# Kernel tuning notes

Hardware: AMD Instinct MI355X
Metric: run time of the kernel (lower is better)

Reference implementation:

```python
import jax, jax.numpy as jnp
import numpy as np

H = 1024
E = 8
TOPK = 2
MLP_H = 4 * H   # resmlp hidden
EXP_H = 2 * H   # expert hidden
EPS_LN = 1e-5


def _ln(x, g, b):
    mu = jnp.mean(x, axis=-1, keepdims=True)
    var = jnp.mean(jnp.square(x - mu), axis=-1, keepdims=True)
    return (x - mu) * jax.lax.rsqrt(var + EPS_LN) * g + b


def setup_inputs() -> dict:
    key = jax.random.key(0)
    ks = jax.random.split(key, 16)
    s = 0.02
    return {
        "x": jax.random.normal(ks[0], (2, 2048, H), jnp.float32),
        # ResidualMLPBlock params
        "ln1_g": jnp.ones((H,), jnp.float32),
        "ln1_b": jnp.zeros((H,), jnp.float32),
        "ln2_g": jnp.ones((H,), jnp.float32),
        "ln2_b": jnp.zeros((H,), jnp.float32),
        "w1": jax.random.normal(ks[1], (H, MLP_H), jnp.float32) * s,
        "b1": jnp.zeros((MLP_H,), jnp.float32),
        "w2": jax.random.normal(ks[2], (MLP_H, H), jnp.float32) * s,
        "b2": jnp.zeros((H,), jnp.float32),
        # MoE params
        "router_w": jax.random.normal(ks[3], (H, E), jnp.float32) * s,
        "ew1": jax.random.normal(ks[4], (E, H, EXP_H), jnp.float32) * s,
        "eb1": jnp.zeros((E, EXP_H), jnp.float32),
        "ew2": jax.random.normal(ks[5], (E, EXP_H, H), jnp.float32) * s,
        "eb2": jnp.zeros((E, H), jnp.float32),
        # final LayerNorm
        "lnf_g": jnp.ones((H,), jnp.float32),
        "lnf_b": jnp.zeros((H,), jnp.float32),
    }


def reference(x, ln1_g, ln1_b, ln2_g, ln2_b, w1, b1, w2, b2,
              router_w, ew1, eb1, ew2, eb2, lnf_g, lnf_b):
    B, L, Hd = x.shape
    # --- ResidualMLPBlock ---
    r = x
    h = _ln(x, ln1_g, ln1_b)
    h = jax.nn.gelu(h @ w1 + b1, approximate=False) @ w2 + b2
    h = h + r
    x = _ln(h, ln2_g, ln2_b) + h
    # --- AdvancedMoEBlock (eval: no dropout / jitter) ---
    xf = x.reshape(-1, Hd)                       # [N, H]
    N = xf.shape[0]
    probs = jax.nn.softmax(xf @ router_w, axis=-1)   # [N, E]
    topk_p, topk_i = jax.lax.top_k(probs, TOPK)      # [N, K]
    topk_p = topk_p / jnp.sum(topk_p, axis=-1, keepdims=True)
    # dense combine weights: w[n, e] = sum_k topk_p[n,k] * [topk_i[n,k]==e]
    comb = jnp.zeros((N, E), xf.dtype).at[jnp.arange(N)[:, None], topk_i].add(topk_p)
    # all-experts dense compute, weighted combine (same math as masked dispatch)
    he = jax.nn.gelu(jnp.einsum('nh,ehf->enf', xf, ew1) + eb1[:, None, :],
                     approximate=False)          # [E, N, 2H]
    ye = jnp.einsum('enf,efh->enh', he, ew2) + eb2[:, None, :]  # [E, N, H]
    out = jnp.einsum('enh,ne->nh', ye, comb).reshape(B, L, Hd)
    # aux load-balancing loss
    counts = jax.ops.segment_sum(jnp.ones((N * TOPK,), jnp.float32),
                                 topk_i.reshape(-1), num_segments=E)
    load = counts / jnp.sum(counts)
    aux_loss = 0.01 * jnp.sum(load * jnp.log(load + 1e-9))
    # --- final LayerNorm ---
    out = _ln(out, lnf_g, lnf_b)
    return out, aux_loss
```

## Files before the change

kernel.cpp:

```cpp
#include <hip/hip_runtime.h>
#include <cstdint>


#define NTOK 4096
#define HD 1024
#define MLPH 4096
#define EXPH 2048
#define NEXP 8
#define KSPLIT 2
#define KCH 2048
#define MAXSLOT 9216

typedef __attribute__((ext_vector_type(8))) _Float16 f16x8;
typedef __attribute__((ext_vector_type(4))) float f32x4v;

__device__ __forceinline__ float gelu_f(float v) {
  return 0.5f * v * (1.0f + erff(v * 0.7071067811865475f));
}

__device__ __forceinline__ void load16_lds(const void* g, void* lds) {
  __builtin_amdgcn_global_load_lds(
      (__attribute__((address_space(1))) unsigned int*)(uintptr_t)g,
      (__attribute__((address_space(3))) unsigned int*)(unsigned)(uintptr_t)lds,
      16, 0, 0);
}

__global__ void transpose_conv2(const float* __restrict__ w1, const float* __restrict__ w2,
                                _Float16* __restrict__ o1, _Float16* __restrict__ o2) {
  __shared__ float t[32][33];
  int z = blockIdx.z;
  const float* in = z ? w2 : w1;
  _Float16* oh = z ? o2 : o1;
  int R = z ? MLPH : HD, C = z ? HD : MLPH;
  int c0 = (z ? blockIdx.y : blockIdx.x) * 32;
  int r0 = (z ? blockIdx.x : blockIdx.y) * 32;
  int tx = threadIdx.x & 31, ty = threadIdx.x >> 5;
#pragma unroll
  for (int i = 0; i < 4; ++i)
    t[ty + i * 8][tx] = in[(size_t)(r0 + ty + i * 8) * C + c0 + tx];
  __syncthreads();
#pragma unroll
  for (int i = 0; i < 4; ++i)
    oh[(size_t)(c0 + ty + i * 8) * R + r0 + tx] = (_Float16)t[tx][ty + i * 8];
}

__global__ void transpose_f16_2(const float* __restrict__ ew1, const float* __restrict__ ew2,
                                _Float16* __restrict__ ew1t, _Float16* __restrict__ ew2t) {
  __shared__ float t[32][33];
  int z = blockIdx.z;
  const float* in;
  _Float16* out;
  int R, C, c0, r0;
  if (z < 8) {
    in = ew1 + (size_t)z * HD * EXPH; out = ew1t + (size_t)z * HD * EXPH;
    R = HD; C = EXPH; c0 = blockIdx.x * 32; r0 = blockIdx.y * 32;
  } else {
    int e = z - 8;
    in = ew2 + (size_t)e * EXPH * HD; out = ew2t + (size_t)e * EXPH * HD;
    R = EXPH; C = HD; c0 = blockIdx.y * 32; r0 = blockIdx.x * 32;
  }
  int tx = threadIdx.x & 31, ty = threadIdx.x >> 5;
#pragma unroll
  for (int i = 0; i < 4; ++i)
    t[ty + i * 8][tx] = in[(size_t)(r0 + ty + i * 8) * C + c0 + tx];
  __syncthreads();
#pragma unroll
  for (int i = 0; i < 4; ++i)
    out[(size_t)(c0 + ty + i * 8) * R + r0 + tx] = (_Float16)t[tx][ty + i * 8];
}

__global__ void ln1_kernel(const float* __restrict__ x, const float* __restrict__ g,
                           const float* __restrict__ b, _Float16* __restrict__ oh) {
  int row = blockIdx.x, tid = threadIdx.x;
  const float4* xr = (const float4*)(x + (size_t)row * HD);
  float4 v = xr[tid];
  float s = v.x + v.y + v.z + v.w;
  float s2 = v.x * v.x + v.y * v.y + v.z * v.z + v.w * v.w;
  __shared__ float red[8];
#pragma unroll
  for (int o = 32; o > 0; o >>= 1) { s += __shfl_xor(s, o, 64); s2 += __shfl_xor(s2, o, 64); }
  if ((tid & 63) == 0) { red[tid >> 6] = s; red[(tid >> 6) + 4] = s2; }
  __syncthreads();
  s = red[0] + red[1] + red[2] + red[3];
  s2 = red[4] + red[5] + red[6] + red[7];
  float mu = s * (1.0f / HD);
  float rstd = 1.0f / sqrtf(s2 * (1.0f / HD) - mu * mu + 1e-5f);
  float4 gv = ((const float4*)g)[tid], bv = ((const float4*)b)[tid];
  size_t base = (size_t)row * HD + tid * 4;
  oh[base + 0] = (_Float16)((v.x - mu) * rstd * gv.x + bv.x);
  oh[base + 1] = (_Float16)((v.y - mu) * rstd * gv.y + bv.y);
  oh[base + 2] = (_Float16)((v.z - mu) * rstd * gv.z + bv.z);
  oh[base + 3] = (_Float16)((v.w - mu) * rstd * gv.w + bv.w);
}

__global__ __launch_bounds__(256, 2) void gemm_f16_gelu(
    const _Float16* __restrict__ A, const _Float16* __restrict__ B,
    const float* __restrict__ bias, _Float16* __restrict__ out, int N, int K) {
  int m0 = blockIdx.y * 128, n0 = blockIdx.x * 128;
  __shared__ __align__(16) _Float16 sA[128 * 64], sB[128 * 64];
  int tid = threadIdx.x, wave = tid >> 6, lane = tid & 63;
  int wm = wave >> 1, wn = wave & 1;
  int r16 = lane & 15, q = lane >> 4;
  f32x4v acc[4][4] = {};
  const _Float16* pA = A + (size_t)m0 * K;
  const _Float16* pB = B + (size_t)n0 * K;
  for (int k0 = 0; k0 < K; k0 += 64) {
    __syncthreads();
#pragma unroll
    for (int i = 0; i < 4; ++i) {
      int s = i * 256 + wave * 64 + lane;
      int row = s >> 3, c2 = s & 7;
      int c2s = c2 ^ (row & 7);
      size_t goff = (size_t)row * K + k0 + c2s * 8;
      int loff = (i * 256 + wave * 64) * 16;
      load16_lds(pA + goff, (char*)sA + loff);
      load16_lds(pB + goff, (char*)sB + loff);
    }
    __syncthreads();
#pragma unroll
    for (int ks = 0; ks < 2; ++ks) {
      f16x8 bf[4];
#pragma unroll
      for (int t = 0; t < 4; ++t) {
        int rowb = wn * 64 + t * 16 + r16;
        bf[t] = *(const f16x8*)&sB[rowb * 64 + ((ks * 4 + q) ^ (rowb & 7)) * 8];
      }
#pragma unroll
      for (int mt = 0; mt < 4; ++mt) {
        int rowa = wm * 64 + mt * 16 + r16;
        f16x8 af = *(const f16x8*)&sA[rowa * 64 + ((ks * 4 + q) ^ (rowa & 7)) * 8];
#pragma unroll
        for (int nt = 0; nt < 4; ++nt)
          acc[mt][nt] = __builtin_amdgcn_mfma_f32_16x16x32_f16(af, bf[nt], acc[mt][nt], 0, 0, 0);
      }
    }
  }
#pragma unroll
  for (int mt = 0; mt < 4; ++mt)
#pragma unroll
    for (int nt = 0; nt < 4; ++nt) {
      int col = n0 + wn * 64 + nt * 16 + r16;
      float bv = bias[col];
#pragma unroll
      for (int r = 0; r < 4; ++r) {
        size_t grow = (size_t)(m0 + wm * 64 + mt * 16 + q * 4 + r);
        out[grow * N + col] = (_Float16)gelu_f(acc[mt][nt][r] + bv);
      }
    }
}

__global__ __launch_bounds__(256, 2) void gemm_f16_pk(
    const _Float16* __restrict__ A, const _Float16* __restrict__ B,
    float* __restrict__ part, int N, int K) {
  int orig = blockIdx.x + 8 * (blockIdx.y + 32 * blockIdx.z);
  int xcd = orig & 7, idx = orig >> 3;
  int wg = xcd * 64 + idx;
  int bz = wg >> 8;
  int rr = wg & 255;
  int by = rr >> 3, bx = rr & 7;
  int m0 = by * 128, n0 = bx * 128;
  int kbase = bz * KCH;
  __shared__ __align__(16) _Float16 sA[128 * 64], sB[128 * 64];
  int tid = threadIdx.x, wave = tid >> 6, lane = tid & 63;
  int wm = wave >> 1, wn = wave & 1;
  int r16 = lane & 15, q = lane >> 4;
  f32x4v acc[4][4] = {};
  const _Float16* pA = A + (size_t)m0 * K + kbase;
  const _Float16* pB = B + (size_t)n0 * K + kbase;
  for (int k0 = 0; k0 < KCH; k0 += 64) {
    __syncthreads();
#pragma unroll
    for (int i = 0; i < 4; ++i) {
      int s = i * 256 + wave * 64 + lane;
      int row = s >> 3, c2 = s & 7;
      int c2s = c2 ^ (row & 7);
      size_t goff = (size_t)row * K + k0 + c2s * 8;
      int loff = (i * 256 + wave * 64) * 16;
      load16_lds(pA + goff, (char*)sA + loff);
      load16_lds(pB + goff, (char*)sB + loff);
    }
    __syncthreads();
#pragma unroll
    for (int ks = 0; ks < 2; ++ks) {
      f16x8 bf[4];
#pragma unroll
      for (int t = 0; t < 4; ++t) {
        int rowb = wn * 64 + t * 16 + r16;
        bf[t] = *(const f16x8*)&sB[rowb * 64 + ((ks * 4 + q) ^ (rowb & 7)) * 8];
      }
#pragma unroll
      for (int mt = 0; mt < 4; ++mt) {
        int rowa = wm * 64 + mt * 16 + r16;
        f16x8 af = *(const f16x8*)&sA[rowa * 64 + ((ks * 4 + q) ^ (rowa & 7)) * 8];
#pragma unroll
        for (int nt = 0; nt < 4; ++nt)
          acc[mt][nt] = __builtin_amdgcn_mfma_f32_16x16x32_f16(af, bf[nt], acc[mt][nt], 0, 0, 0);
      }
    }
  }
  float* pz = part + (size_t)bz * NTOK * HD;
#pragma unroll
  for (int mt = 0; mt < 4; ++mt)
#pragma unroll
    for (int nt = 0; nt < 4; ++nt) {
      int col = n0 + wn * 64 + nt * 16 + r16;
#pragma unroll
      for (int r = 0; r < 4; ++r) {
        size_t grow = (size_t)(m0 + wm * 64 + mt * 16 + q * 4 + r);
        pz[grow * N + col] = acc[mt][nt][r];
      }
    }
}

__global__ void reduce_ln2_router_kernel(
    const float* __restrict__ part, const float* __restrict__ x,
    const float* __restrict__ b2, const float* __restrict__ g,
    const float* __restrict__ b, const float* __restrict__ rw,
    _Float16* __restrict__ x2h, int* __restrict__ tidx, float* __restrict__ twt,
    int* __restrict__ counts) {
  int row = blockIdx.x, tid = threadIdx.x;
  int lane = tid & 63, wid = tid >> 6;
  float4 v = {0, 0, 0, 0};
#pragma unroll
  for (int z = 0; z < KSPLIT; ++z) {
    float4 p = ((const float4*)(part + ((size_t)z * NTOK + row) * HD))[tid];
    v.x += p.x; v.y += p.y; v.z += p.z; v.w += p.w;
  }
  float4 bb = ((const float4*)b2)[tid];
  float4 xv = ((const float4*)(x + (size_t)row * HD))[tid];
  v.x += bb.x + xv.x; v.y += bb.y + xv.y; v.z += bb.z + xv.z; v.w += bb.w + xv.w;
  float s = v.x + v.y + v.z + v.w;
  float s2 = v.x * v.x + v.y * v.y + v.z * v.z + v.w * v.w;
  __shared__ float red[8];
  __shared__ float sred[4][8];
#pragma unroll
  for (int o = 32; o > 0; o >>= 1) { s += __shfl_xor(s, o, 64); s2 += __shfl_xor(s2, o, 64); }
  if (lane == 0) { red[wid] = s; red[wid + 4] = s2; }
  __syncthreads();
  s = red[0] + red[1] + red[2] + red[3];
  s2 = red[4] + red[5] + red[6] + red[7];
  float mu = s * (1.0f / HD);
  float rstd = 1.0f / sqrtf(s2 * (1.0f / HD) - mu * mu + 1e-5f);
  float4 gv = ((const float4*)g)[tid], bv = ((const float4*)b)[tid];
  float4 o4;
  o4.x = (v.x - mu) * rstd * gv.x + bv.x + v.x;
  o4.y = (v.y - mu) * rstd * gv.y + bv.y + v.y;
  o4.z = (v.z - mu) * rstd * gv.z + bv.z + v.z;
  o4.w = (v.w - mu) * rstd * gv.w + bv.w + v.w;
  size_t base = (size_t)row * HD + tid * 4;
  x2h[base + 0] = (_Float16)o4.x;
  x2h[base + 1] = (_Float16)o4.y;
  x2h[base + 2] = (_Float16)o4.z;
  x2h[base + 3] = (_Float16)o4.w;
  float lg[8] = {0, 0, 0, 0, 0, 0, 0, 0};
  {
    const float4* rp = (const float4*)(rw + (size_t)tid * 32);
    float xc[4] = {o4.x, o4.y, o4.z, o4.w};
#pragma unroll
    for (int jj = 0; jj < 4; ++jj) {
      float4 r0 = rp[jj * 2], r1 = rp[jj * 2 + 1];
      lg[0] += xc[jj] * r0.x; lg[1] += xc[jj] * r0.y;
      lg[2] += xc[jj] * r0.z; lg[3] += xc[jj] * r0.w;
      lg[4] += xc[jj] * r1.x; lg[5] += xc[jj] * r1.y;
      lg[6] += xc[jj] * r1.z; lg[7] += xc[jj] * r1.w;
    }
  }
#pragma unroll
  for (int o = 32; o > 0; o >>= 1)
#pragma unroll
    for (int e = 0; e < 8; ++e) lg[e] += __shfl_xor(lg[e], o, 64);
  if (lane == 0)
#pragma unroll
    for (int e = 0; e < 8; ++e) sred[wid][e] = lg[e];
  __syncthreads();
  if (tid == 0) {
    float l8[8];
#pragma unroll
    for (int e = 0; e < 8; ++e)
      l8[e] = sred[0][e] + sred[1][e] + sred[2][e] + sred[3][e];
    int e0 = 0; float m0v = l8[0];
#pragma unroll
    for (int e = 1; e < 8; ++e) if (l8[e] > m0v) { m0v = l8[e]; e0 = e; }
    int e1 = -1; float m1v = -3.4e38f;
#pragma unroll
    for (int e = 0; e < 8; ++e) if (e != e0 && l8[e] > m1v) { m1v = l8[e]; e1 = e; }
    float p0 = 1.0f / (1.0f + expf(m1v - m0v));
    tidx[2 * row] = e0; tidx[2 * row + 1] = e1;
    twt[2 * row] = p0; twt[2 * row + 1] = 1.0f - p0;
    atomicAdd(&counts[e0], 1);
    atomicAdd(&counts[e1], 1);
  }
}

__global__ void route_block(const int* __restrict__ counts, const int* __restrict__ tidx,
                            int* __restrict__ poff_g, float* __restrict__ auxp,
                            int* __restrict__ slotmap, int* __restrict__ slot2token) {
  __shared__ int poff[9];
  __shared__ int cur[8];
  int tid = threadIdx.x;
  if (tid == 0) {
    int acc = 0; poff[0] = 0; float aux = 0.0f;
    for (int e = 0; e < NEXP; ++e) {
      int c = counts[e];
      float load = (float)c / (float)(NTOK * 2);
      aux += load * logf(load + 1e-9f);
      acc += ((c + 127) >> 7) << 7;
      poff[e + 1] = acc;
    }
    auxp[0] = 0.01f * aux;
  }
  if (tid < 8) cur[tid] = 0;
  __syncthreads();
  for (int t = tid; t < NTOK; t += 256) {
#pragma unroll
    for (int k = 0; k < 2; ++k) {
      int e = tidx[2 * t + k];
      int slot = poff[e] + atomicAdd(&cur[e], 1);
      slotmap[2 * t + k] = slot;
      slot2token[slot] = t;
    }
  }
  __syncthreads();
  for (int e = 0; e < NEXP; ++e) {
    int lo = poff[e] + counts[e], hi = poff[e + 1];
    for (int s2 = lo + tid; s2 < hi; s2 += 256) slot2token[s2] = 0;
  }
  if (tid < 9) poff_g[tid] = poff[tid];
}

template <int EPI>
__global__ __launch_bounds__(256, 2) void gemm_expert(
    const _Float16* __restrict__ A, const _Float16* __restrict__ B,
    const float* __restrict__ bias, void* __restrict__ out,
    int N, int K, const int* __restrict__ poff, size_t bstride, int bias_stride,
    const int* __restrict__ s2t) {
  int e = blockIdx.z;
  int lo = poff[e], hi = poff[e + 1];
  int m0 = lo + blockIdx.y * 128;
  if (m0 >= hi) return;
  const _Float16* Bt = B + (size_t)e * bstride;
  const float* bias_e = bias + (size_t)e * bias_stride;
  int n0 = blockIdx.x * 128;
  __shared__ __align__(16) _Float16 sA[128 * 64];
  __shared__ __align__(16) _Float16 sB[128 * 64];
  int tid = threadIdx.x, wave = tid >> 6, lane = tid & 63;
  int wm = wave >> 1, wn = wave & 1;
  int r16 = lane & 15, q = lane >> 4;
  f32x4v acc[4][4] = {};
  size_t aoff[4]; size_t boff[4];
#pragma unroll
  for (int i = 0; i < 4; ++i) {
    int s = i * 256 + wave * 64 + lane;
    int row = s >> 3, c2 = s & 7;
    int c2s = c2 ^ (row & 7);
    int am = m0 + row;
    size_t arow = (EPI == 0) ? (size_t)s2t[am] : (size_t)am;
    aoff[i] = arow * K + c2s * 8;
    boff[i] = (size_t)(n0 + row) * K + c2s * 8;
  }
  for (int k0 = 0; k0 < K; k0 += 64) {
    __syncthreads();
#pragma unroll
    for (int i = 0; i < 4; ++i) {
      int loff = (i * 256 + wave * 64) * 16;
      load16_lds(A + aoff[i] + k0, (char*)sA + loff);
      load16_lds(Bt + boff[i] + k0, (char*)sB + loff);
    }
    __syncthreads();
#pragma unroll
    for (int ks = 0; ks < 2; ++ks) {
      f16x8 bf[4];
#pragma unroll
      for (int t = 0; t < 4; ++t) {
        int rowb = wn * 64 + t * 16 + r16;
        bf[t] = *(const f16x8*)&sB[rowb * 64 + ((ks * 4 + q) ^ (rowb & 7)) * 8];
      }
#pragma unroll
      for (int mt = 0; mt < 4; ++mt) {
        int rowa = wm * 64 + mt * 16 + r16;
        f16x8 af = *(const f16x8*)&sA[rowa * 64 + ((ks * 4 + q) ^ (rowa & 7)) * 8];
#pragma unroll
        for (int nt = 0; nt < 4; ++nt)
          acc[mt][nt] = __builtin_amdgcn_mfma_f32_16x16x32_f16(af, bf[nt], acc[mt][nt], 0, 0, 0);
      }
    }
  }
#pragma unroll
  for (int mt = 0; mt < 4; ++mt)
#pragma unroll
    for (int nt = 0; nt < 4; ++nt) {
      int col = n0 + wn * 64 + nt * 16 + r16;
      float bv = bias_e[col];
#pragma unroll
      for (int r = 0; r < 4; ++r) {
        size_t grow = (size_t)(m0 + wm * 64 + mt * 16 + q * 4 + r);
        float v = acc[mt][nt][r] + bv;
        if (EPI == 0)
          ((_Float16*)out)[grow * N + col] = (_Float16)gelu_f(v);
        else
          ((float*)out)[grow * N + col] = v;
      }
    }
}

__global__ void combine_ln_kernel(const float* __restrict__ ybuf, const int* __restrict__ slotmap,
                                  const float* __restrict__ twt, const float* __restrict__ g,
                                  const float* __restrict__ b, float* __restrict__ out) {
  int t = blockIdx.x, tid = threadIdx.x;
  int s0 = slotmap[2 * t], s1 = slotmap[2 * t + 1];
  float w0 = twt[2 * t], w1 = twt[2 * t + 1];
  float4 a = ((const float4*)(ybuf + (size_t)s0 * HD))[tid];
  float4 c = ((const float4*)(ybuf + (size_t)s1 * HD))[tid];
  float4 v;
  v.x = w0 * a.x + w1 * c.x; v.y = w0 * a.y + w1 * c.y;
  v.z = w0 * a.z + w1 * c.z; v.w = w0 * a.w + w1 * c.w;
  float s = v.x + v.y + v.z + v.w;
  float s2 = v.x * v.x + v.y * v.y + v.z * v.z + v.w * v.w;
  __shared__ float red[8];
#pragma unroll
  for (int o = 32; o > 0; o >>= 1) { s += __shfl_xor(s, o, 64); s2 += __shfl_xor(s2, o, 64); }
  if ((tid & 63) == 0) { red[tid >> 6] = s; red[(tid >> 6) + 4] = s2; }
  __syncthreads();
  s = red[0] + red[1] + red[2] + red[3];
  s2 = red[4] + red[5] + red[6] + red[7];
  float mu = s * (1.0f / HD);
  float rstd = 1.0f / sqrtf(s2 * (1.0f / HD) - mu * mu + 1e-5f);
  float4 gv = ((const float4*)g)[tid], bv = ((const float4*)b)[tid];
  float4 o4;
  o4.x = (v.x - mu) * rstd * gv.x + bv.x;
  o4.y = (v.y - mu) * rstd * gv.y + bv.y;
  o4.z = (v.z - mu) * rstd * gv.z + bv.z;
  o4.w = (v.w - mu) * rstd * gv.w + bv.w;
  ((float4*)(out + (size_t)t * HD))[tid] = o4;
}

extern "C" void kernel_launch(void* const* d_in, const int* in_sizes, int n_in,
                              void* d_out, int out_size, void* d_ws, size_t ws_size,
                              hipStream_t stream) {
  const float* x    = (const float*)d_in[0];
  const float* ln1g = (const float*)d_in[1];
  const float* ln1b = (const float*)d_in[2];
  const float* ln2g = (const float*)d_in[3];
  const float* ln2b = (const float*)d_in[4];
  const float* w1   = (const float*)d_in[5];
  const float* b1   = (const float*)d_in[6];
  const float* w2   = (const float*)d_in[7];
  const float* b2   = (const float*)d_in[8];
  const float* rw   = (const float*)d_in[9];
  const float* ew1  = (const float*)d_in[10];
  const float* eb1  = (const float*)d_in[11];
  const float* ew2  = (const float*)d_in[12];
  const float* eb2  = (const float*)d_in[13];
  const float* lnfg = (const float*)d_in[14];
  const float* lnfb = (const float*)d_in[15];

  char* ws = (char*)d_ws;
  _Float16* acth = (_Float16*)(ws + 0);
  _Float16* ew2t = (_Float16*)(ws + 0);
  _Float16* ew1t = (_Float16*)(ws + 33554432);
  _Float16* w1th = (_Float16*)(ws + 67108864);
  _Float16* x2h  = (_Float16*)(ws + 67108864);
  _Float16* w2th = (_Float16*)(ws + 75497472);
  _Float16* h1h  = (_Float16*)(ws + 100663296);
  float*    part = (float*)(ws + 100663296);
  float*    ybuf = (float*)(ws + 100663296);
  _Float16* a1   = (_Float16*)(ws + 167772160);
  const size_t offS = 205520896;
  int*   counts     = (int*)(ws + offS);
  int*   poff       = (int*)(ws + offS + 64);
  int*   tidx       = (int*)(ws + offS + 1024);
  float* twt        = (float*)(ws + offS + 1024 + 32768);
  int*   slotmap    = (int*)(ws + offS + 1024 + 65536);
  int*   slot2token = (int*)(ws + offS + 1024 + 98304);

  float* out  = (float*)d_out;
  float* auxp = out + (size_t)NTOK * HD;

  dim3 b256(256);
  hipMemsetAsync(ws + offS, 0, 64, stream);

  transpose_conv2<<<dim3(128, 32, 2), b256, 0, stream>>>(w1, w2, w1th, w2th);

  ln1_kernel<<<NTOK, b256, 0, stream>>>(x, ln1g, ln1b, h1h);
  gemm_f16_gelu<<<dim3(MLPH / 128, NTOK / 128, 1), b256, 0, stream>>>(
      h1h, w1th, b1, acth, MLPH, HD);
  gemm_f16_pk<<<dim3(HD / 128, NTOK / 128, KSPLIT), b256, 0, stream>>>(
      acth, w2th, part, HD, MLPH);
  reduce_ln2_router_kernel<<<NTOK, b256, 0, stream>>>(
      part, x, b2, ln2g, ln2b, rw, x2h, tidx, twt, counts);

  transpose_f16_2<<<dim3(64, 32, 16), b256, 0, stream>>>(ew1, ew2, ew1t, ew2t);

  route_block<<<1, b256, 0, stream>>>(counts, tidx, poff, auxp, slotmap, slot2token);

  gemm_expert<0><<<dim3(EXPH / 128, NTOK / 128, NEXP), b256, 0, stream>>>(
      x2h, ew1t, eb1, a1, EXPH, HD, poff, (size_t)EXPH * HD, EXPH, slot2token);
  gemm_expert<1><<<dim3(HD / 128, NTOK / 128, NEXP), b256, 0, stream>>>(
      a1, ew2t, eb2, ybuf, HD, EXPH, poff, (size_t)HD * EXPH, HD, nullptr);

  combine_ln_kernel<<<NTOK, b256, 0, stream>>>(ybuf, slotmap, twt, lnfg, lnfb, out);
}
```

Before: 554.5 us.

## Parallelize MoE routing into histogram, offset scan, and scatter kernels

Replaces the single-block routing kernel and the global atomic expert counters with a three-stage scheme: per-chunk histograms over 64 blocks, a single-block scan that computes padded expert offsets, per-chunk bases and the aux loss, then a parallel scatter that assigns slots. This removes 4096×2 global atomics from the LN2/router kernel, the memset, and the serial single-block slot assignment. It adds two extra kernel launches, and slot order within an expert becomes chunk-ordered.

```diff
diff --git a/kernel.cpp b/kernel.cpp
--- a/kernel.cpp
+++ b/kernel.cpp
@@ -10,6 +10,7 @@
 #define KSPLIT 2
 #define KCH 2048
 #define MAXSLOT 9216
+#define NCH 64
 
 typedef __attribute__((ext_vector_type(8))) _Float16 f16x8;
 typedef __attribute__((ext_vector_type(4))) float f32x4v;
@@ -216,8 +217,7 @@
     const float* __restrict__ part, const float* __restrict__ x,
     const float* __restrict__ b2, const float* __restrict__ g,
     const float* __restrict__ b, const float* __restrict__ rw,
-    _Float16* __restrict__ x2h, int* __restrict__ tidx, float* __restrict__ twt,
-    int* __restrict__ counts) {
+    _Float16* __restrict__ x2h, int* __restrict__ tidx, float* __restrict__ twt) {
   int row = blockIdx.x, tid = threadIdx.x;
   int lane = tid & 63, wid = tid >> 6;
   float4 v = {0, 0, 0, 0};
@@ -287,21 +287,40 @@
     float p0 = 1.0f / (1.0f + expf(m1v - m0v));
     tidx[2 * row] = e0; tidx[2 * row + 1] = e1;
     twt[2 * row] = p0; twt[2 * row + 1] = 1.0f - p0;
-    atomicAdd(&counts[e0], 1);
-    atomicAdd(&counts[e1], 1);
-  }
-}
-
-__global__ void route_block(const int* __restrict__ counts, const int* __restrict__ tidx,
-                            int* __restrict__ poff_g, float* __restrict__ auxp,
-                            int* __restrict__ slotmap, int* __restrict__ slot2token) {
+  }
+}
+
+__global__ void route_hist(const int* __restrict__ tidx, int* __restrict__ cpart) {
+  __shared__ int c8[8];
+  int b = blockIdx.x, tid = threadIdx.x;
+  if (tid < 8) c8[tid] = 0;
+  __syncthreads();
+  int e = tidx[b * (NTOK * 2 / NCH) + tid];
+  atomicAdd(&c8[e], 1);
+  __syncthreads();
+  if (tid < 8) cpart[b * 8 + tid] = c8[tid];
+}
+
+__global__ void route_offsets(const int* __restrict__ cpart,
+                              int* __restrict__ poff_g, float* __restrict__ auxp,
+                              int* __restrict__ cbase, int* __restrict__ slot2token) {
+  __shared__ int sc[NCH * 8];
+  __shared__ int cnt8[8];
   __shared__ int poff[9];
-  __shared__ int cur[8];
   int tid = threadIdx.x;
+  sc[tid] = cpart[tid];
+  sc[tid + 256] = cpart[tid + 256];
+  __syncthreads();
+  if (tid < 8) {
+    int acc = 0;
+    for (int b = 0; b < NCH; ++b) acc += sc[b * 8 + tid];
+    cnt8[tid] = acc;
+  }
+  __syncthreads();
   if (tid == 0) {
     int acc = 0; poff[0] = 0; float aux = 0.0f;
     for (int e = 0; e < NEXP; ++e) {
-      int c = counts[e];
+      int c = cnt8[e];
       float load = (float)c / (float)(NTOK * 2);
       aux += load * logf(load + 1e-9f);
       acc += ((c + 127) >> 7) << 7;
@@ -309,23 +328,32 @@
     }
     auxp[0] = 0.01f * aux;
   }
-  if (tid < 8) cur[tid] = 0;
-  __syncthreads();
-  for (int t = tid; t < NTOK; t += 256) {
-#pragma unroll
-    for (int k = 0; k < 2; ++k) {
-      int e = tidx[2 * t + k];
-      int slot = poff[e] + atomicAdd(&cur[e], 1);
-      slotmap[2 * t + k] = slot;
-      slot2token[slot] = t;
-    }
-  }
-  __syncthreads();
+  __syncthreads();
+  if (tid < 8) {
+    int acc = poff[tid];
+    for (int b = 0; b < NCH; ++b) {
+      cbase[b * 8 + tid] = acc;
+      acc += sc[b * 8 + tid];
+    }
+  }
   for (int e = 0; e < NEXP; ++e) {
-    int lo = poff[e] + counts[e], hi = poff[e + 1];
+    int lo = poff[e] + cnt8[e], hi = poff[e + 1];
     for (int s2 = lo + tid; s2 < hi; s2 += 256) slot2token[s2] = 0;
   }
   if (tid < 9) poff_g[tid] = poff[tid];
+}
+
+__global__ void route_scatter(const int* __restrict__ tidx, const int* __restrict__ cbase,
+                              int* __restrict__ slotmap, int* __restrict__ slot2token) {
+  __shared__ int cur[8];
+  int b = blockIdx.x, tid = threadIdx.x;
+  if (tid < 8) cur[tid] = cbase[b * 8 + tid];
+  __syncthreads();
+  int i = b * (NTOK * 2 / NCH) + tid;
+  int e = tidx[i];
+  int slot = atomicAdd(&cur[e], 1);
+  slotmap[i] = slot;
+  slot2token[slot] = i >> 1;
 }
 
 template <int EPI>
@@ -466,18 +494,18 @@
   float*    ybuf = (float*)(ws + 100663296);
   _Float16* a1   = (_Float16*)(ws + 167772160);
   const size_t offS = 205520896;
-  int*   counts     = (int*)(ws + offS);
   int*   poff       = (int*)(ws + offS + 64);
   int*   tidx       = (int*)(ws + offS + 1024);
   float* twt        = (float*)(ws + offS + 1024 + 32768);
   int*   slotmap    = (int*)(ws + offS + 1024 + 65536);
   int*   slot2token = (int*)(ws + offS + 1024 + 98304);
+  int*   cpart      = (int*)(ws + offS + 1024 + 98304 + 36864);
+  int*   cbase      = (int*)(ws + offS + 1024 + 98304 + 36864 + 2048);
 
   float* out  = (float*)d_out;
   float* auxp = out + (size_t)NTOK * HD;
 
   dim3 b256(256);
-  hipMemsetAsync(ws + offS, 0, 64, stream);
 
   transpose_conv2<<<dim3(128, 32, 2), b256, 0, stream>>>(w1, w2, w1th, w2th);
 
@@ -487,11 +515,13 @@
   gemm_f16_pk<<<dim3(HD / 128, NTOK / 128, KSPLIT), b256, 0, stream>>>(
       acth, w2th, part, HD, MLPH);
   reduce_ln2_router_kernel<<<NTOK, b256, 0, stream>>>(
-      part, x, b2, ln2g, ln2b, rw, x2h, tidx, twt, counts);
+      part, x, b2, ln2g, ln2b, rw, x2h, tidx, twt);
+
+  route_hist<<<NCH, dim3(128), 0, stream>>>(tidx, cpart);
+  route_offsets<<<1, b256, 0, stream>>>(cpart, poff, auxp, cbase, slot2token);
+  route_scatter<<<NCH, dim3(128), 0, stream>>>(tidx, cbase, slotmap, slot2token);
 
   transpose_f16_2<<<dim3(64, 32, 16), b256, 0, stream>>>(ew1, ew2, ew1t, ew2t);
-
-  route_block<<<1, b256, 0, stream>>>(counts, tidx, poff, auxp, slotmap, slot2token);
 
   gemm_expert<0><<<dim3(EXPH / 128, NTOK / 128, NEXP), b256, 0, stream>>>(
       x2h, ew1t, eb1, a1, EXPH, HD, poff, (size_t)EXPH * HD, EXPH, slot2token);
```

Result: faster. 481.1 us (-13.2%).
